# Optimization experiments

Measured on AMD Instinct MI355X. Metric: run time of the kernel, lower is better.

The kernel has to match this reference:

```python
import jax, jax.numpy as jnp
from jax import lax
import numpy as np

SIGMAS = (30.0, 150.0, 300.0)
RESTORE_FACTOR = 2.0
COLOR_GAIN = 10.0
GAIN = 270.0
OFFSET = 128.0
EPS = 1e-6


def _dwconv(x, k2d, stride):
    # depthwise 2D conv, NCHW, VALID padding (caller pads)
    C = x.shape[1]
    kh, kw = k2d.shape
    w = jnp.broadcast_to(k2d.astype(x.dtype)[None, None], (C, 1, kh, kw))
    return lax.conv_general_dilated(
        x, w, (stride, stride), 'VALID',
        dimension_numbers=('NCHW', 'OIHW', 'NCHW'),
        feature_group_count=C)


def _pyr_down(x):
    # cv2.pyrDown: 5x5 binomial kernel, reflect-101 border, stride-2 decimation
    k1 = jnp.array([1., 4., 6., 4., 1.], jnp.float32) / 16.0
    k2 = jnp.outer(k1, k1)
    xp = jnp.pad(x, ((0, 0), (0, 0), (2, 2), (2, 2)), mode='reflect')
    return _dwconv(xp, k2, 2)


def _gauss_blur(x, ksize):
    # cv2.GaussianBlur with sigmaX=0: sigma derived from kernel size
    s = 0.3 * ((ksize - 1) * 0.5 - 1.0) + 0.8
    i = jnp.arange(ksize, dtype=jnp.float32) - (ksize - 1) / 2.0
    g = jnp.exp(-(i * i) / (2.0 * s * s))
    g = g / g.sum()
    k2 = jnp.outer(g, g)
    p = ksize // 2
    xp = jnp.pad(x, ((0, 0), (0, 0), (p, p), (p, p)), mode='reflect')
    return _dwconv(xp, k2, 1)


def _fast_filter(x, sigma):
    # Faithful port of GaussianBlurConv.FastFilter (static Python recursion:
    # sigma is a compile-time constant, so depth is fixed at trace time).
    sigma = min(sigma, 300.0)
    k = int(round(sigma * 3 * 2 + 1)) | 1
    if k < 3:
        return x
    if k < 10:
        return _gauss_blur(x, k)
    h, w = x.shape[2], x.shape[3]
    if h < 2 or w < 2:
        return x
    sub = _fast_filter(_pyr_down(x), sigma / 2.0)
    # cv2.resize default INTER_LINEAR == half-pixel bilinear
    return jax.image.resize(sub, (x.shape[0], x.shape[1], h, w), method='bilinear')


def _msr_forward(x):
    img = x * 255.0 + 1.0                      # (N,3,H,W)
    log_img = jnp.log10(img + EPS)
    retinex = sum(log_img - jnp.log10(_fast_filter(img, s) + EPS) for s in SIGMAS)
    retinex = retinex / len(SIGMAS)
    img_sum = jnp.sum(img, axis=1, keepdims=True)   # (N,1,H,W)
    color_rest = jnp.log10(img * RESTORE_FACTOR / (img_sum + EPS) + 1.0)
    enhanced = retinex * color_rest * COLOR_GAIN * GAIN + OFFSET
    return jnp.clip(enhanced, 0.0, 255.0) / 255.0


def setup_inputs() -> dict:
    key = jax.random.key(0)
    x = jax.random.uniform(key, (8, 3, 1280, 1280), dtype=jnp.float32)
    return {"x": x}


def reference(x):
    return _msr_forward(x)
```

## Files before the change

kernel.cpp:

```cpp
#include <hip/hip_runtime.h>

#define NC 24

typedef float f32x4 __attribute__((ext_vector_type(4)));

__device__ __forceinline__ float pyr_point(const float* ip, int Hi, int Wi, int oy, int ox)
{
    const float k1[5] = {0.0625f, 0.25f, 0.375f, 0.25f, 0.0625f};
    float acc = 0.f;
#pragma unroll
    for (int i = 0; i < 5; ++i) {
        int y = 2 * oy - 2 + i;
        y = (y < 0) ? -y : y;
        y = (y >= Hi) ? (2 * Hi - 2 - y) : y;
        const float* rp = ip + (size_t)y * Wi;
        float r = 0.f;
#pragma unroll
        for (int j = 0; j < 5; ++j) {
            int xx = 2 * ox - 2 + j;
            xx = (xx < 0) ? -xx : xx;
            xx = (xx >= Wi) ? (2 * Wi - 2 - xx) : xx;
            r = fmaf(k1[j], rp[xx], r);
        }
        acc = fmaf(k1[i], r, acc);
    }
    return acc;
}

template <int K>
__device__ __forceinline__ float blur_point(const float* ip, int H, int W, int oy, int ox,
                                            const float* w)
{
    const int R = K / 2;
    float acc = 0.f;
#pragma unroll
    for (int i = 0; i < K; ++i) {
        int y = oy - R + i;
        y = (y < 0) ? -y : y;
        y = (y >= H) ? (2 * H - 2 - y) : y;
        const float* rp = ip + (size_t)y * W;
        float r = 0.f;
#pragma unroll
        for (int j = 0; j < K; ++j) {
            int xx = ox - R + j;
            xx = (xx < 0) ? -xx : xx;
            xx = (xx >= W) ? (2 * W - 2 - xx) : xx;
            r = fmaf(w[j], rp[xx], r);
        }
        acc = fmaf(w[i], r, acc);
    }
    return acc;
}

__global__ void __launch_bounds__(256) pyrdown_lds_kernel(
    const float* __restrict__ in, float* __restrict__ out,
    int Hi, int Wi, int Ho, int Wo, float scale, float offs)
{
    const int TW = 132;
    __shared__ float vs[16 * TW];
    const int tid = threadIdx.x;
    const int OX = blockIdx.x * 64;
    const int OY = blockIdx.y * 16;
    const int nc = blockIdx.z;
    const float k1[5] = {0.0625f, 0.25f, 0.375f, 0.25f, 0.0625f};
    const float* ip = in + (size_t)nc * Hi * Wi;

    for (int idx = tid; idx < 16 * TW; idx += 256) {
        int r = idx / TW;
        int c = idx - r * TW;
        int oy = OY + r;
        if (oy >= Ho) oy = Ho - 1;
        int xc = 2 * OX - 2 + c;
        xc = (xc < 0) ? -xc : xc;
        xc = (xc >= Wi) ? (2 * Wi - 2 - xc) : xc;
        xc = max(0, min(Wi - 1, xc));
        float acc = 0.f;
#pragma unroll
        for (int i = 0; i < 5; ++i) {
            int y = 2 * oy - 2 + i;
            y = (y < 0) ? -y : y;
            y = (y >= Hi) ? (2 * Hi - 2 - y) : y;
            acc = fmaf(k1[i], ip[(size_t)y * Wi + xc], acc);
        }
        vs[idx] = acc;
    }
    __syncthreads();

    for (int o = tid; o < 1024; o += 256) {
        int r = o >> 6, c = o & 63;
        int ox = OX + c, oy = OY + r;
        if (ox >= Wo || oy >= Ho) continue;
        const float* vp = &vs[r * TW + 2 * c];
        float s = 0.f;
#pragma unroll
        for (int j = 0; j < 5; ++j) s = fmaf(k1[j], vp[j], s);
        out[((size_t)nc * Ho + oy) * Wo + ox] = fmaf(s, scale, offs);
    }
}

__global__ void __launch_bounds__(256) base_kernel(
    const float* __restrict__ L4g, float* __restrict__ b30g,
    float* __restrict__ b150g, float* __restrict__ b300g)
{
    __shared__ float sL4[80 * 80];
    __shared__ float sL5[40 * 40];
    __shared__ float sL6[20 * 20];
    __shared__ float sL7[10 * 10];
    __shared__ float sL8[5 * 5];
    const int nc = blockIdx.x;
    const int tid = threadIdx.x;

    float w7[7], w9[9];
    {
        float s = 1.4f, s2 = 2.f * s * s, sum = 0.f;
#pragma unroll
        for (int i = 0; i < 7; ++i) { float d = (float)i - 3.f; w7[i] = expf(-(d * d) / s2); sum += w7[i]; }
#pragma unroll
        for (int i = 0; i < 7; ++i) w7[i] /= sum;
        s = 1.7f; s2 = 2.f * s * s; sum = 0.f;
#pragma unroll
        for (int i = 0; i < 9; ++i) { float d = (float)i - 4.f; w9[i] = expf(-(d * d) / s2); sum += w9[i]; }
#pragma unroll
        for (int i = 0; i < 9; ++i) w9[i] /= sum;
    }

    const float* src = L4g + (size_t)nc * 6400;
    for (int i = tid; i < 1600; i += 256)
        *(f32x4*)&sL4[4 * i] = *(const f32x4*)&src[4 * i];
    __syncthreads();
    for (int i = tid; i < 1600; i += 256) {
        int oy = i / 40, ox = i - oy * 40;
        sL5[i] = pyr_point(sL4, 80, 80, oy, ox);
    }
    __syncthreads();
    for (int i = tid; i < 400; i += 256) {
        int oy = i / 20, ox = i - oy * 20;
        sL6[i] = pyr_point(sL5, 40, 40, oy, ox);
    }
    __syncthreads();
    for (int i = tid; i < 100; i += 256) {
        int oy = i / 10, ox = i - oy * 10;
        sL7[i] = pyr_point(sL6, 20, 20, oy, ox);
    }
    __syncthreads();
    for (int i = tid; i < 25; i += 256) {
        int oy = i / 5, ox = i - oy * 5;
        sL8[i] = pyr_point(sL7, 10, 10, oy, ox);
    }
    __syncthreads();
    for (int i = tid; i < 1600; i += 256) {
        int oy = i / 40, ox = i - oy * 40;
        b30g[(size_t)nc * 1600 + i] = blur_point<7>(sL5, 40, 40, oy, ox, w7);
    }
    for (int i = tid; i < 100; i += 256) {
        int oy = i / 10, ox = i - oy * 10;
        b150g[(size_t)nc * 100 + i] = blur_point<9>(sL7, 10, 10, oy, ox, w9);
    }
    for (int i = tid; i < 25; i += 256) {
        int oy = i / 5, ox = i - oy * 5;
        b300g[(size_t)nc * 25 + i] = blur_point<9>(sL8, 5, 5, oy, ox, w9);
    }
}

__global__ void __launch_bounds__(256) mega_final(
    const float* __restrict__ x,
    const float* __restrict__ b30g,
    const float* __restrict__ b150g,
    const float* __restrict__ b300g,
    float* __restrict__ out)
{
    const int H = 1280, W = 1280;
    __shared__ float S[3 * 1963];

    const int tid = threadIdx.x;
    const int X0 = blockIdx.x * 64, Y0 = blockIdx.y * 64;
    const int n = blockIdx.z;

    const int LS[7] = {320, 160, 80, 40, 20, 10, 5};
    int ay[7], by[7], ax[7], bx[7];
    ay[0] = max(0, Y0 / 4 - 1); by[0] = min(319, Y0 / 4 + 16);
    ax[0] = max(0, X0 / 4 - 1); bx[0] = min(319, X0 / 4 + 16);
#pragma unroll
    for (int l = 1; l < 7; ++l) {
        ay[l] = max(0, (ay[l - 1] >> 1) - 1); by[l] = min(LS[l] - 1, (by[l - 1] >> 1) + 1);
        ax[l] = max(0, (ax[l - 1] >> 1) - 1); bx[l] = min(LS[l] - 1, (bx[l - 1] >> 1) + 1);
    }
    const int o300t[7] = {1639, 1495, 1414, 1365, 1329, 1293, 1268};
    const int o150t[6] = {944, 800, 719, 670, 634, 598};
    const int o30t[4]  = {274, 130, 49, 0};

    {
        int ny = by[3] - ay[3] + 1, nx = bx[3] - ax[3] + 1;
        for (int i = tid; i < 3 * ny * nx; i += 256) {
            int c = i / (ny * nx), pt = i - c * (ny * nx);
            int ry = pt / nx, rx = pt - ry * nx;
            S[c * 1963 + o30t[3] + pt] =
                b30g[(size_t)(n * 3 + c) * 1600 + (ay[3] + ry) * 40 + ax[3] + rx];
        }
        ny = by[5] - ay[5] + 1; nx = bx[5] - ax[5] + 1;
        for (int i = tid; i < 3 * ny * nx; i += 256) {
            int c = i / (ny * nx), pt = i - c * (ny * nx);
            int ry = pt / nx, rx = pt - ry * nx;
            S[c * 1963 + o150t[5] + pt] =
                b150g[(size_t)(n * 3 + c) * 100 + (ay[5] + ry) * 10 + ax[5] + rx];
        }
        ny = by[6] - ay[6] + 1; nx = bx[6] - ax[6] + 1;
        for (int i = tid; i < 3 * ny * nx; i += 256) {
            int c = i / (ny * nx), pt = i - c * (ny * nx);
            int ry = pt / nx, rx = pt - ry * nx;
            S[c * 1963 + o300t[6] + pt] =
                b300g[(size_t)(n * 3 + c) * 25 + (ay[6] + ry) * 5 + ax[6] + rx];
        }
    }
    __syncthreads();

#pragma unroll
    for (int l = 5; l >= 0; --l) {
        int srcO[9], dstO[9];
        int m = 0;
#pragma unroll
        for (int c = 0; c < 3; ++c) { srcO[m] = c * 1963 + o300t[l + 1]; dstO[m] = c * 1963 + o300t[l]; ++m; }
        if (l <= 4) {
#pragma unroll
            for (int c = 0; c < 3; ++c) { srcO[m] = c * 1963 + o150t[l + 1]; dstO[m] = c * 1963 + o150t[l]; ++m; }
        }
        if (l <= 2) {
#pragma unroll
            for (int c = 0; c < 3; ++c) { srcO[m] = c * 1963 + o30t[l + 1]; dstO[m] = c * 1963 + o30t[l]; ++m; }
        }
        int ny = by[l] - ay[l] + 1, nx = bx[l] - ax[l] + 1;
        int nxS = bx[l + 1] - ax[l + 1] + 1;
        int Ssrc = LS[l + 1];
        int npts = ny * nx;
        for (int i = tid; i < m * npts; i += 256) {
            int p = i / npts, pt = i - p * npts;
            int ry = pt / nx, rx = pt - ry * nx;
            int oy = ay[l] + ry, ox = ax[l] + rx;
            int my = oy >> 1, py = oy & 1;
            int mx = ox >> 1, px = ox & 1;
            int yA = py ? my : max(my - 1, 0);
            int yB = py ? min(my + 1, Ssrc - 1) : my;
            float wyA = py ? 0.75f : 0.25f, wyB = py ? 0.25f : 0.75f;
            int xA = px ? mx : max(mx - 1, 0);
            int xB = px ? min(mx + 1, Ssrc - 1) : mx;
            float wxA = px ? 0.75f : 0.25f, wxB = px ? 0.25f : 0.75f;
            const float* sp = &S[srcO[p]];
            int la = (yA - ay[l + 1]) * nxS - ax[l + 1];
            int lb = (yB - ay[l + 1]) * nxS - ax[l + 1];
            float v = wyA * (wxA * sp[la + xA] + wxB * sp[la + xB]) +
                      wyB * (wxA * sp[lb + xA] + wxB * sp[lb + xB]);
            S[dstO[p] + pt] = v;
        }
        __syncthreads();
    }

    int tyi = tid >> 4, txi = tid & 15;
    int byi = Y0 / 4 + tyi, bxi = X0 / 4 + txi;
    int nx0 = bx[0] - ax[0] + 1;
    int ry[3], rx[3];
    ry[0] = (byi > 0 ? byi - 1 : 0) - ay[0]; ry[1] = byi - ay[0];
    ry[2] = (byi < 319 ? byi + 1 : 319) - ay[0];
    rx[0] = (bxi > 0 ? bxi - 1 : 0) - ax[0]; rx[1] = bxi - ax[0];
    rx[2] = (bxi < 319 ? bxi + 1 : 319) - ax[0];
    const int ol0[3] = {274, 944, 1639};

    f32x4 xi[3][4];
#pragma unroll
    for (int c = 0; c < 3; ++c)
#pragma unroll
        for (int qy = 0; qy < 4; ++qy)
            xi[c][qy] = __builtin_nontemporal_load(
                (const f32x4*)&x[((size_t)(n * 3 + c) * H + 4 * byi + qy) * W + 4 * bxi]);

    float crcp[4][4];
#pragma unroll
    for (int qy = 0; qy < 4; ++qy)
#pragma unroll
        for (int qx = 0; qx < 4; ++qx) {
            float s = (xi[0][qy][qx] + xi[1][qy][qx] + xi[2][qy][qx]) * 255.f + 3.f;
            crcp[qy][qx] = __fdividef(2.f, s + 1e-6f);
        }

#pragma unroll
    for (int c = 0; c < 3; ++c) {
        float prod[4][4];
#pragma unroll
        for (int qy = 0; qy < 4; ++qy)
#pragma unroll
            for (int qx = 0; qx < 4; ++qx) prod[qy][qx] = 1.f;

#pragma unroll
        for (int s = 0; s < 3; ++s) {
            const float* fp = &S[c * 1963 + ol0[s]];
            float v[3][3];
#pragma unroll
            for (int i = 0; i < 3; ++i)
#pragma unroll
                for (int j = 0; j < 3; ++j) v[i][j] = fp[ry[i] * nx0 + rx[j]];
            float cy[4][3];
#pragma unroll
            for (int j = 0; j < 3; ++j) {
                float v0 = v[0][j], v1 = v[1][j], v2 = v[2][j];
                cy[0][j] = fmaf(0.375f, v0, 0.625f * v1);
                cy[1][j] = fmaf(0.1875f, v0, fmaf(0.75f, v1, 0.0625f * v2));
                cy[2][j] = fmaf(0.0625f, v0, fmaf(0.75f, v1, 0.1875f * v2));
                cy[3][j] = fmaf(0.625f, v1, 0.375f * v2);
            }
#pragma unroll
            for (int qy = 0; qy < 4; ++qy) {
                float a0 = cy[qy][0], a1 = cy[qy][1], a2 = cy[qy][2];
                float t0 = fmaf(0.375f, a0, 0.625f * a1);
                float t1 = fmaf(0.1875f, a0, fmaf(0.75f, a1, 0.0625f * a2));
                float t2 = fmaf(0.0625f, a0, fmaf(0.75f, a1, 0.1875f * a2));
                float t3 = fmaf(0.625f, a1, 0.375f * a2);
                prod[qy][0] *= (t0 + 1e-6f);
                prod[qy][1] *= (t1 + 1e-6f);
                prod[qy][2] *= (t2 + 1e-6f);
                prod[qy][3] *= (t3 + 1e-6f);
            }
        }

#pragma unroll
        for (int qy = 0; qy < 4; ++qy) {
            f32x4 o;
#pragma unroll
            for (int qx = 0; qx < 4; ++qx) {
                float img = xi[c][qy][qx] * 255.f + 1.f;
                float a = img + 1e-6f;
                float l2a = __log2f(__fdividef(a * a * a, prod[qy][qx]));
                float carg = fmaf(img, crcp[qy][qx], 1.f);
                float l2c = __log2f(carg);
                float e = fmaf(l2a * l2c, 81.55715246f, 128.f);
                e = fminf(fmaxf(e, 0.f), 255.f);
                o[qx] = e * (1.f / 255.f);
            }
            __builtin_nontemporal_store(
                o, (f32x4*)&out[((size_t)(n * 3 + c) * H + 4 * byi + qy) * W + 4 * bxi]);
        }
    }
}

extern "C" void kernel_launch(void* const* d_in, const int* in_sizes, int n_in,
                              void* d_out, int out_size, void* d_ws, size_t ws_size,
                              hipStream_t stream)
{
    const float* x = (const float*)d_in[0];
    float* out = (float*)d_out;
    float* ws = (float*)d_ws;

    size_t off = 0;
    auto alloc = [&](int d) { float* p = ws + off; off += (size_t)NC * d * d; return p; };
    float* L1 = alloc(640);
    float* L2 = alloc(320);
    float* L3 = alloc(160);
    float* L4 = alloc(80);
    float* b30 = alloc(40);
    float* b150 = alloc(10);
    float* b300 = alloc(5);
    (void)ws_size; (void)in_sizes; (void)n_in; (void)out_size;

    dim3 blk(256, 1, 1);
    auto gridP = [&](int Wo, int Ho) { return dim3((Wo + 63) / 64, (Ho + 15) / 16, NC); };

    pyrdown_lds_kernel<<<gridP(640, 640), blk, 0, stream>>>(x,  L1, 1280, 1280, 640, 640, 255.f, 1.f);
    pyrdown_lds_kernel<<<gridP(320, 320), blk, 0, stream>>>(L1, L2, 640, 640, 320, 320, 1.f, 0.f);
    pyrdown_lds_kernel<<<gridP(160, 160), blk, 0, stream>>>(L2, L3, 320, 320, 160, 160, 1.f, 0.f);
    pyrdown_lds_kernel<<<gridP(80,  80),  blk, 0, stream>>>(L3, L4, 160, 160, 80, 80, 1.f, 0.f);
    base_kernel<<<dim3(NC, 1, 1), dim3(256, 1, 1), 0, stream>>>(L4, b30, b150, b300);
    mega_final<<<dim3(20, 20, 8), dim3(256, 1, 1), 0, stream>>>(x, b30, b150, b300, out);
}
```

Baseline: 390.0 us.

## Use fixed-size clamped tile windows and templated upsample levels in final kernel

Replaces the data-dependent per-level window bounds with fixed-size windows whose coordinates are clamped at image edges. This lets each upsample level be a template with compile-time sizes, so index divisions become constant and the loads for all planes at a point share one set of address computations. The initial loads of the blurred coarse levels are split across thread groups by fixed offsets, and the shared-memory footprint shrinks. The goal is less integer index arithmetic and fewer loop iterations in the block-local pyramid upsampling, at the cost of redundant clamped duplicates at borders.

```diff
diff --git a/kernel.cpp b/kernel.cpp
--- a/kernel.cpp
+++ b/kernel.cpp
@@ -162,6 +162,60 @@
     }
 }
 
+#define CH 1721
+#define O30_3 0
+#define O30_2 36
+#define O30_1 100
+#define O30_0 244
+#define O150_5 568
+#define O150_4 593
+#define O150_3 618
+#define O150_2 654
+#define O150_1 718
+#define O150_0 862
+#define O300_6 1186
+#define O300_5 1211
+#define O300_4 1236
+#define O300_3 1261
+#define O300_2 1297
+#define O300_1 1333
+#define O300_0 1397
+
+template <int NPL, int ND, int NS, int LSD>
+__device__ __forceinline__ void up_level(float* __restrict__ S,
+                                         const int (&srcO)[NPL], const int (&dstO)[NPL],
+                                         int ayD, int axD, int ayS, int axS)
+{
+    const int SSRC = LSD / 2;
+    const int NPTS = ND * ND;
+    for (int pt = threadIdx.x; pt < NPTS; pt += 256) {
+        int ry = pt / ND, rx = pt - ry * ND;
+        int gy = min(max(ayD + ry, 0), LSD - 1);
+        int gx = min(max(axD + rx, 0), LSD - 1);
+        int my = gy >> 1, py = gy & 1;
+        int mx = gx >> 1, px = gx & 1;
+        int yA = py ? my : max(my - 1, 0);
+        int yB = py ? min(my + 1, SSRC - 1) : my;
+        float wyA = py ? 0.75f : 0.25f;
+        float wyB = 1.0f - wyA;
+        int xA = px ? mx : max(mx - 1, 0);
+        int xB = px ? min(mx + 1, SSRC - 1) : mx;
+        float wxA = px ? 0.75f : 0.25f;
+        float wxB = 1.0f - wxA;
+        int la = (yA - ayS) * NS + (xA - axS);
+        int laB = la + (xB - xA);
+        int lb = (yB - ayS) * NS + (xA - axS);
+        int lbB = lb + (xB - xA);
+#pragma unroll
+        for (int p = 0; p < NPL; ++p) {
+            const float* sp = S + srcO[p];
+            float v = wyA * fmaf(wxA, sp[la], wxB * sp[laB]) +
+                      wyB * fmaf(wxA, sp[lb], wxB * sp[lbB]);
+            S[dstO[p] + pt] = v;
+        }
+    }
+}
+
 __global__ void __launch_bounds__(256) mega_final(
     const float* __restrict__ x,
     const float* __restrict__ b30g,
@@ -170,99 +224,96 @@
     float* __restrict__ out)
 {
     const int H = 1280, W = 1280;
-    __shared__ float S[3 * 1963];
+    __shared__ float S[3 * CH];
 
     const int tid = threadIdx.x;
     const int X0 = blockIdx.x * 64, Y0 = blockIdx.y * 64;
     const int n = blockIdx.z;
 
-    const int LS[7] = {320, 160, 80, 40, 20, 10, 5};
-    int ay[7], by[7], ax[7], bx[7];
-    ay[0] = max(0, Y0 / 4 - 1); by[0] = min(319, Y0 / 4 + 16);
-    ax[0] = max(0, X0 / 4 - 1); bx[0] = min(319, X0 / 4 + 16);
+    int ay[7], ax[7];
+    ay[0] = (Y0 >> 2) - 1;
+    ax[0] = (X0 >> 2) - 1;
 #pragma unroll
     for (int l = 1; l < 7; ++l) {
-        ay[l] = max(0, (ay[l - 1] >> 1) - 1); by[l] = min(LS[l] - 1, (by[l - 1] >> 1) + 1);
-        ax[l] = max(0, (ax[l - 1] >> 1) - 1); bx[l] = min(LS[l] - 1, (bx[l - 1] >> 1) + 1);
-    }
-    const int o300t[7] = {1639, 1495, 1414, 1365, 1329, 1293, 1268};
-    const int o150t[6] = {944, 800, 719, 670, 634, 598};
-    const int o30t[4]  = {274, 130, 49, 0};
-
-    {
-        int ny = by[3] - ay[3] + 1, nx = bx[3] - ax[3] + 1;
-        for (int i = tid; i < 3 * ny * nx; i += 256) {
-            int c = i / (ny * nx), pt = i - c * (ny * nx);
-            int ry = pt / nx, rx = pt - ry * nx;
-            S[c * 1963 + o30t[3] + pt] =
-                b30g[(size_t)(n * 3 + c) * 1600 + (ay[3] + ry) * 40 + ax[3] + rx];
-        }
-        ny = by[5] - ay[5] + 1; nx = bx[5] - ax[5] + 1;
-        for (int i = tid; i < 3 * ny * nx; i += 256) {
-            int c = i / (ny * nx), pt = i - c * (ny * nx);
-            int ry = pt / nx, rx = pt - ry * nx;
-            S[c * 1963 + o150t[5] + pt] =
-                b150g[(size_t)(n * 3 + c) * 100 + (ay[5] + ry) * 10 + ax[5] + rx];
-        }
-        ny = by[6] - ay[6] + 1; nx = bx[6] - ax[6] + 1;
-        for (int i = tid; i < 3 * ny * nx; i += 256) {
-            int c = i / (ny * nx), pt = i - c * (ny * nx);
-            int ry = pt / nx, rx = pt - ry * nx;
-            S[c * 1963 + o300t[6] + pt] =
-                b300g[(size_t)(n * 3 + c) * 25 + (ay[6] + ry) * 5 + ax[6] + rx];
-        }
-    }
-    __syncthreads();
-
-#pragma unroll
-    for (int l = 5; l >= 0; --l) {
-        int srcO[9], dstO[9];
-        int m = 0;
-#pragma unroll
-        for (int c = 0; c < 3; ++c) { srcO[m] = c * 1963 + o300t[l + 1]; dstO[m] = c * 1963 + o300t[l]; ++m; }
-        if (l <= 4) {
-#pragma unroll
-            for (int c = 0; c < 3; ++c) { srcO[m] = c * 1963 + o150t[l + 1]; dstO[m] = c * 1963 + o150t[l]; ++m; }
-        }
-        if (l <= 2) {
-#pragma unroll
-            for (int c = 0; c < 3; ++c) { srcO[m] = c * 1963 + o30t[l + 1]; dstO[m] = c * 1963 + o30t[l]; ++m; }
-        }
-        int ny = by[l] - ay[l] + 1, nx = bx[l] - ax[l] + 1;
-        int nxS = bx[l + 1] - ax[l + 1] + 1;
-        int Ssrc = LS[l + 1];
-        int npts = ny * nx;
-        for (int i = tid; i < m * npts; i += 256) {
-            int p = i / npts, pt = i - p * npts;
-            int ry = pt / nx, rx = pt - ry * nx;
-            int oy = ay[l] + ry, ox = ax[l] + rx;
-            int my = oy >> 1, py = oy & 1;
-            int mx = ox >> 1, px = ox & 1;
-            int yA = py ? my : max(my - 1, 0);
-            int yB = py ? min(my + 1, Ssrc - 1) : my;
-            float wyA = py ? 0.75f : 0.25f, wyB = py ? 0.25f : 0.75f;
-            int xA = px ? mx : max(mx - 1, 0);
-            int xB = px ? min(mx + 1, Ssrc - 1) : mx;
-            float wxA = px ? 0.75f : 0.25f, wxB = px ? 0.25f : 0.75f;
-            const float* sp = &S[srcO[p]];
-            int la = (yA - ay[l + 1]) * nxS - ax[l + 1];
-            int lb = (yB - ay[l + 1]) * nxS - ax[l + 1];
-            float v = wyA * (wxA * sp[la + xA] + wxB * sp[la + xB]) +
-                      wyB * (wxA * sp[lb + xA] + wxB * sp[lb + xB]);
-            S[dstO[p] + pt] = v;
-        }
-        __syncthreads();
-    }
+        ay[l] = (ay[l - 1] >> 1) - 1;
+        ax[l] = (ax[l - 1] >> 1) - 1;
+    }
+
+    if (tid < 36) {
+        int ry = tid / 6, rx = tid - ry * 6;
+        int gy = min(max(ay[3] + ry, 0), 39);
+        int gx = min(max(ax[3] + rx, 0), 39);
+#pragma unroll
+        for (int c = 0; c < 3; ++c)
+            S[c * CH + O30_3 + tid] = b30g[(size_t)(n * 3 + c) * 1600 + gy * 40 + gx];
+    } else if (tid >= 64 && tid < 89) {
+        int t = tid - 64;
+        int ry = t / 5, rx = t - ry * 5;
+        int gy = min(max(ay[5] + ry, 0), 9);
+        int gx = min(max(ax[5] + rx, 0), 9);
+#pragma unroll
+        for (int c = 0; c < 3; ++c)
+            S[c * CH + O150_5 + t] = b150g[(size_t)(n * 3 + c) * 100 + gy * 10 + gx];
+    } else if (tid >= 128 && tid < 153) {
+        int t = tid - 128;
+        int ry = t / 5, rx = t - ry * 5;
+        int gy = min(max(ay[6] + ry, 0), 4);
+        int gx = min(max(ax[6] + rx, 0), 4);
+#pragma unroll
+        for (int c = 0; c < 3; ++c)
+            S[c * CH + O300_6 + t] = b300g[(size_t)(n * 3 + c) * 25 + gy * 5 + gx];
+    }
+    __syncthreads();
+
+    {
+        const int s[3] = {O300_6, O300_6 + CH, O300_6 + 2 * CH};
+        const int d[3] = {O300_5, O300_5 + CH, O300_5 + 2 * CH};
+        up_level<3, 5, 5, 10>(S, s, d, ay[5], ax[5], ay[6], ax[6]);
+    }
+    __syncthreads();
+    {
+        const int s[6] = {O300_5, O300_5 + CH, O300_5 + 2 * CH, O150_5, O150_5 + CH, O150_5 + 2 * CH};
+        const int d[6] = {O300_4, O300_4 + CH, O300_4 + 2 * CH, O150_4, O150_4 + CH, O150_4 + 2 * CH};
+        up_level<6, 5, 5, 20>(S, s, d, ay[4], ax[4], ay[5], ax[5]);
+    }
+    __syncthreads();
+    {
+        const int s[6] = {O300_4, O300_4 + CH, O300_4 + 2 * CH, O150_4, O150_4 + CH, O150_4 + 2 * CH};
+        const int d[6] = {O300_3, O300_3 + CH, O300_3 + 2 * CH, O150_3, O150_3 + CH, O150_3 + 2 * CH};
+        up_level<6, 6, 5, 40>(S, s, d, ay[3], ax[3], ay[4], ax[4]);
+    }
+    __syncthreads();
+    {
+        const int s[9] = {O300_3, O300_3 + CH, O300_3 + 2 * CH, O150_3, O150_3 + CH, O150_3 + 2 * CH,
+                          O30_3, O30_3 + CH, O30_3 + 2 * CH};
+        const int d[9] = {O300_2, O300_2 + CH, O300_2 + 2 * CH, O150_2, O150_2 + CH, O150_2 + 2 * CH,
+                          O30_2, O30_2 + CH, O30_2 + 2 * CH};
+        up_level<9, 8, 6, 80>(S, s, d, ay[2], ax[2], ay[3], ax[3]);
+    }
+    __syncthreads();
+    {
+        const int s[9] = {O300_2, O300_2 + CH, O300_2 + 2 * CH, O150_2, O150_2 + CH, O150_2 + 2 * CH,
+                          O30_2, O30_2 + CH, O30_2 + 2 * CH};
+        const int d[9] = {O300_1, O300_1 + CH, O300_1 + 2 * CH, O150_1, O150_1 + CH, O150_1 + 2 * CH,
+                          O30_1, O30_1 + CH, O30_1 + 2 * CH};
+        up_level<9, 12, 8, 160>(S, s, d, ay[1], ax[1], ay[2], ax[2]);
+    }
+    __syncthreads();
+    {
+        const int s[9] = {O300_1, O300_1 + CH, O300_1 + 2 * CH, O150_1, O150_1 + CH, O150_1 + 2 * CH,
+                          O30_1, O30_1 + CH, O30_1 + 2 * CH};
+        const int d[9] = {O300_0, O300_0 + CH, O300_0 + 2 * CH, O150_0, O150_0 + CH, O150_0 + 2 * CH,
+                          O30_0, O30_0 + CH, O30_0 + 2 * CH};
+        up_level<9, 18, 12, 320>(S, s, d, ay[0], ax[0], ay[1], ax[1]);
+    }
+    __syncthreads();
 
     int tyi = tid >> 4, txi = tid & 15;
-    int byi = Y0 / 4 + tyi, bxi = X0 / 4 + txi;
-    int nx0 = bx[0] - ax[0] + 1;
+    int byi = (Y0 >> 2) + tyi, bxi = (X0 >> 2) + txi;
     int ry[3], rx[3];
-    ry[0] = (byi > 0 ? byi - 1 : 0) - ay[0]; ry[1] = byi - ay[0];
-    ry[2] = (byi < 319 ? byi + 1 : 319) - ay[0];
-    rx[0] = (bxi > 0 ? bxi - 1 : 0) - ax[0]; rx[1] = bxi - ax[0];
-    rx[2] = (bxi < 319 ? bxi + 1 : 319) - ax[0];
-    const int ol0[3] = {274, 944, 1639};
+    ry[0] = max(byi - 1, 0) - ay[0]; ry[1] = byi - ay[0]; ry[2] = min(byi + 1, 319) - ay[0];
+    rx[0] = max(bxi - 1, 0) - ax[0]; rx[1] = bxi - ax[0]; rx[2] = min(bxi + 1, 319) - ax[0];
+    const int ol0[3] = {O30_0, O150_0, O300_0};
 
     f32x4 xi[3][4];
 #pragma unroll
@@ -291,12 +342,12 @@
 
 #pragma unroll
         for (int s = 0; s < 3; ++s) {
-            const float* fp = &S[c * 1963 + ol0[s]];
+            const float* fp = &S[c * CH + ol0[s]];
             float v[3][3];
 #pragma unroll
             for (int i = 0; i < 3; ++i)
 #pragma unroll
-                for (int j = 0; j < 3; ++j) v[i][j] = fp[ry[i] * nx0 + rx[j]];
+                for (int j = 0; j < 3; ++j) v[i][j] = fp[ry[i] * 18 + rx[j]];
             float cy[4][3];
 #pragma unroll
             for (int j = 0; j < 3; ++j) {
```

New measurement: 356.2 us. 8.7% less time.
